# Performance work log

Measured on AMD Instinct MI355X. Metric: run time of the kernel, lower is better.

## Reference

```python
import jax, jax.numpy as jnp
import numpy as np

N, C_DEC, H, W = 16, 512, 32, 32
C_ENC, S, FEATS_IN, N_HEAD = 768, 77, 512, 8
EPS = 1e-5


def setup_inputs() -> dict:
    key = jax.random.key(0)
    ks = jax.random.split(key, 12)
    inp = {
        "input": jax.random.normal(ks[0], (N, C_DEC, H, W), jnp.float32),
        "cond": jax.random.normal(ks[1], (N, FEATS_IN), jnp.float32),
        "enc_hidden": jax.random.normal(ks[2], (N, S, C_ENC), jnp.float32),
        "enc_padding_mask": jax.random.randint(ks[3], (N, S), 0, 2).astype(jnp.float32),
        # AdaGN linear: feats_in -> 2*c_dec (scales, shifts)
        "adagn_w": jax.random.normal(ks[4], (2 * C_DEC, FEATS_IN), jnp.float32) * 0.02,
        "adagn_b": jnp.zeros((2 * C_DEC,), jnp.float32),
        # LayerNorm(c_enc) affine
        "ln_w": jnp.ones((C_ENC,), jnp.float32),
        "ln_b": jnp.zeros((C_ENC,), jnp.float32),
        # 1x1 conv q projection (treated as channel matmul)
        "q_w": jax.random.normal(ks[5], (C_DEC, C_DEC), jnp.float32) * 0.02,
        "q_b": jnp.zeros((C_DEC,), jnp.float32),
        # kv linear: c_enc -> 2*c_dec
        "kv_w": jax.random.normal(ks[6], (2 * C_DEC, C_ENC), jnp.float32) * 0.02,
        "kv_b": jnp.zeros((2 * C_DEC,), jnp.float32),
        # 1x1 conv out projection
        "out_w": jax.random.normal(ks[7], (C_DEC, C_DEC), jnp.float32) * 0.02,
        "out_b": jnp.zeros((C_DEC,), jnp.float32),
    }
    return inp


def reference(input, cond, enc_hidden, enc_padding_mask,
              adagn_w, adagn_b, ln_w, ln_b,
              q_w, q_b, kv_w, kv_b, out_w, out_b):
    n, c, h, w = input.shape
    d = c // N_HEAD

    # --- AdaGN: GroupNorm(1, c, affine=False) then cond-dependent scale/shift ---
    mu = jnp.mean(input, axis=(1, 2, 3), keepdims=True)
    var = jnp.var(input, axis=(1, 2, 3), keepdims=True)
    normed = (input - mu) * jax.lax.rsqrt(var + EPS)
    ss = cond @ adagn_w.T + adagn_b                      # [n, 2c]
    scales, shifts = ss[:, :c], ss[:, c:]
    x = shifts[:, :, None, None] + normed * (scales[:, :, None, None] + 1.0)

    # --- q projection (1x1 conv == per-pixel channel matmul) ---
    q = jnp.einsum('nchw,oc->nohw', x, q_w) + q_b[None, :, None, None]
    q = q.reshape(n, N_HEAD, d, h * w).transpose(0, 1, 3, 2)   # [n, head, hw, d]

    # --- encoder LayerNorm + kv projection ---
    mu_e = jnp.mean(enc_hidden, axis=-1, keepdims=True)
    var_e = jnp.var(enc_hidden, axis=-1, keepdims=True)
    e = (enc_hidden - mu_e) * jax.lax.rsqrt(var_e + EPS) * ln_w + ln_b
    kv = e @ kv_w.T + kv_b                               # [n, S, 2c]
    s = kv.shape[1]
    kv = kv.reshape(n, s, 2 * N_HEAD, d).transpose(0, 2, 1, 3)  # [n, 2*head, S, d]
    k, v = kv[:, :N_HEAD], kv[:, N_HEAD:]

    # --- scaled dot-product attention with additive padding mask ---
    scale = d ** (-0.25)
    att = jnp.einsum('nhqd,nhkd->nhqk', q * scale, k * scale)
    att = att - enc_padding_mask[:, None, None, :] * 10000.0
    att = jax.nn.softmax(att, axis=-1)
    y = jnp.einsum('nhqk,nhkd->nhqd', att, v)            # [n, head, hw, d]
    y = y.transpose(0, 1, 3, 2).reshape(n, c, h, w)

    out = jnp.einsum('nchw,oc->nohw', y, out_w) + out_b[None, :, None, None]
    return input + out
```

## Files before the change

### kernel.cpp

```cpp
#include <hip/hip_runtime.h>
#include <math.h>

typedef unsigned short u16;
typedef __bf16 bf16x8 __attribute__((ext_vector_type(8)));
typedef float f32x4 __attribute__((ext_vector_type(4)));

#define AS1 __attribute__((address_space(1)))
#define AS3 __attribute__((address_space(3)))

#define N_    16
#define C_    512
#define HW_   1024
#define CE_   768
#define S_    77
#define NH_   8
#define D_    64
#define FEATS_ 512
#define EPS_  1e-5f
#define TOK_  (N_ * S_)

#define WS_PSTAT 0
#define WS_QBIAS 1024
#define WSU_BYTE 131072
#define U_QW  0
#define U_OW  262144
#define U_KVW 524288
#define U_EB  1310720
#define U_KVB 2256896
#define U_QT  3518464
#define U_XT  11907072

__device__ __forceinline__ u16 f2bf(float f) {
    unsigned u = __float_as_uint(f);
    return (u16)((u + 0x7FFFu + ((u >> 16) & 1u)) >> 16);
}
__device__ __forceinline__ float bf2f(u16 h) {
    return __uint_as_float(((unsigned)h) << 16);
}

__global__ __launch_bounds__(256) void mega1_kernel(const float* __restrict__ inp,
                                                    float* __restrict__ pstats,
                                                    const float* __restrict__ qw,
                                                    const float* __restrict__ ow,
                                                    const float* __restrict__ kvw,
                                                    u16* __restrict__ uq,
                                                    u16* __restrict__ uo,
                                                    u16* __restrict__ ukv,
                                                    const float* __restrict__ enc,
                                                    const float* __restrict__ lnw,
                                                    const float* __restrict__ lnb,
                                                    u16* __restrict__ eb,
                                                    const float* __restrict__ cond,
                                                    const float* __restrict__ agw,
                                                    const float* __restrict__ agb,
                                                    float* __restrict__ ssf) {
    int bid = blockIdx.x;
    int tid = threadIdx.x;
    if (bid < 256) {
        int n = bid >> 4, slice = bid & 15;
        const float* base = inp + (size_t)n * C_ * HW_ + slice * (C_ * HW_ / 16);
        float s = 0.f, s2 = 0.f;
        const float4* b4 = (const float4*)base;
        for (int i = tid; i < (C_ * HW_ / 16) / 4; i += 256) {
            float4 v = b4[i];
            s  += v.x + v.y + v.z + v.w;
            s2 += v.x * v.x + v.y * v.y + v.z * v.z + v.w * v.w;
        }
        for (int off = 32; off; off >>= 1) {
            s  += __shfl_down(s, off);
            s2 += __shfl_down(s2, off);
        }
        __shared__ float sh[8];
        int wid = tid >> 6, lane = tid & 63;
        if (lane == 0) { sh[wid] = s; sh[4 + wid] = s2; }
        __syncthreads();
        if (tid == 0) {
            pstats[bid * 2]     = sh[0] + sh[1] + sh[2] + sh[3];
            pstats[bid * 2 + 1] = sh[4] + sh[5] + sh[6] + sh[7];
        }
    } else if (bid < 1536) {
        int i = (bid - 256) * 256 + tid;
        const float* s; u16* d; int j;
        if (i < 65536)       { s = qw;  d = uq;  j = i; }
        else if (i < 131072) { s = ow;  d = uo;  j = i - 65536; }
        else                 { s = kvw; d = ukv; j = i - 131072; }
        float4 v = ((const float4*)s)[j];
        ushort4 w;
        w.x = f2bf(v.x); w.y = f2bf(v.y); w.z = f2bf(v.z); w.w = f2bf(v.w);
        ((ushort4*)(d))[j] = w;
    } else if (bid < 2768) {
        int tok = bid - 1536;
        const float* row = enc + (size_t)tok * CE_;
        int t = tid;
        float v0 = row[t], v1 = row[t + 256], v2 = row[t + 512];
        float sum = v0 + v1 + v2;
        float sq  = v0 * v0 + v1 * v1 + v2 * v2;
        for (int off = 32; off; off >>= 1) {
            sum += __shfl_down(sum, off);
            sq  += __shfl_down(sq, off);
        }
        __shared__ float red[8];
        int wid = t >> 6, lane = t & 63;
        if (lane == 0) { red[wid] = sum; red[4 + wid] = sq; }
        __syncthreads();
        float tot = red[0] + red[1] + red[2] + red[3];
        float tsq = red[4] + red[5] + red[6] + red[7];
        float mu  = tot / CE_;
        float var = tsq / CE_ - mu * mu;
        float rstd = rsqrtf(var + EPS_);
        u16* o = eb + (size_t)tok * CE_;
        o[t]       = f2bf((v0 - mu) * rstd * lnw[t] + lnb[t]);
        o[t + 256] = f2bf((v1 - mu) * rstd * lnw[t + 256] + lnb[t + 256]);
        o[t + 512] = f2bf((v2 - mu) * rstd * lnw[t + 512] + lnb[t + 512]);
    } else {
        __shared__ float wz[16][512];
        __shared__ float cz[16][512];
        int r0 = (bid - 2768) * 16;
        for (int i = tid; i < 2048; i += 256) {
            int row = i >> 7, f4 = i & 127;
            *(float4*)&cz[row][f4 * 4] = ((const float4*)(cond + (size_t)row * 512))[f4];
            *(float4*)&wz[row][f4 * 4] = ((const float4*)(agw + (size_t)(r0 + row) * 512))[f4];
        }
        __syncthreads();
        int n = tid >> 4, r = tid & 15;
        float acc = agb[r0 + r];
        for (int i = 0; i < 128; i++) {
            int j = (r + i) & 127;
            float4 c4 = *(const float4*)&cz[n][j * 4];
            float4 w4 = *(const float4*)&wz[r][j * 4];
            acc += c4.x * w4.x + c4.y * w4.y + c4.z * w4.z + c4.w * w4.w;
        }
        ssf[(size_t)n * 1024 + r0 + r] = acc;
    }
}

__global__ __launch_bounds__(256) void mega2_kernel(const float* __restrict__ inp,
                                                    const float* __restrict__ ssf,
                                                    const float* __restrict__ pstats,
                                                    u16* __restrict__ xT,
                                                    const float* __restrict__ qw,
                                                    const float* __restrict__ qb,
                                                    float* __restrict__ qbias) {
    int bid = blockIdx.x;
    int tid = threadIdx.x;
    float cnt = (float)(C_ * HW_);
    if (bid < 2048) {
        int n = bid >> 7, rem = bid & 127;
        int c0 = (rem >> 4) * 64, h0 = (rem & 15) * 64;
        float s = 0.f, s2 = 0.f;
        for (int k = 0; k < 16; k++) {
            s  += pstats[(n * 16 + k) * 2];
            s2 += pstats[(n * 16 + k) * 2 + 1];
        }
        float mu = s / cnt;
        float rstd = rsqrtf(s2 / cnt - mu * mu + EPS_);
        __shared__ float t[64][65];
        int rr = tid >> 4, cc = (tid & 15) * 4;
#pragma unroll
        for (int i = 0; i < 4; i++) {
            int cl = rr + i * 16;
            int c = c0 + cl;
            float a = rstd * (ssf[(size_t)n * 1024 + c] + 1.f);
            float4 v = *(const float4*)(inp + ((size_t)n * C_ + c) * HW_ + h0 + cc);
            t[cl][cc + 0] = v.x * a; t[cl][cc + 1] = v.y * a;
            t[cl][cc + 2] = v.z * a; t[cl][cc + 3] = v.w * a;
        }
        __syncthreads();
#pragma unroll
        for (int i = 0; i < 4; i++) {
            int hl = rr + i * 16;
            ushort4 w;
            w.x = f2bf(t[cc + 0][hl]); w.y = f2bf(t[cc + 1][hl]);
            w.z = f2bf(t[cc + 2][hl]); w.w = f2bf(t[cc + 3][hl]);
            *(ushort4*)(xT + ((size_t)n * HW_ + h0 + hl) * C_ + c0 + cc) = w;
        }
    } else {
        __shared__ float wz[16][512];
        __shared__ float cz[16][512];
        __shared__ float muS[16], rsS[16];
        int r0 = (bid - 2048) * 16;
        if (tid < 16) {
            float s = 0.f, s2 = 0.f;
            for (int k = 0; k < 16; k++) {
                s  += pstats[(tid * 16 + k) * 2];
                s2 += pstats[(tid * 16 + k) * 2 + 1];
            }
            float mu = s / cnt;
            muS[tid] = mu;
            rsS[tid] = rsqrtf(s2 / cnt - mu * mu + EPS_);
        }
        __syncthreads();
        for (int i = tid; i < 2048; i += 256) {
            int row = i >> 7, f4 = i & 127;
            float4 sc4 = ((const float4*)(ssf + (size_t)row * 1024))[f4];
            float4 sh4 = ((const float4*)(ssf + (size_t)row * 1024 + 512))[f4];
            float mu = muS[row], rs = rsS[row];
            float4 b;
            b.x = sh4.x - mu * (rs * (sc4.x + 1.f));
            b.y = sh4.y - mu * (rs * (sc4.y + 1.f));
            b.z = sh4.z - mu * (rs * (sc4.z + 1.f));
            b.w = sh4.w - mu * (rs * (sc4.w + 1.f));
            *(float4*)&cz[row][f4 * 4] = b;
            *(float4*)&wz[row][f4 * 4] = ((const float4*)(qw + (size_t)(r0 + row) * 512))[f4];
        }
        __syncthreads();
        int n = tid >> 4, r = tid & 15;
        float acc = qb[r0 + r];
        for (int i = 0; i < 128; i++) {
            int j = (r + i) & 127;
            float4 c4 = *(const float4*)&cz[n][j * 4];
            float4 w4 = *(const float4*)&wz[r][j * 4];
            acc += c4.x * w4.x + c4.y * w4.y + c4.z * w4.z + c4.w * w4.w;
        }
        qbias[(size_t)n * 512 + r0 + r] = acc;
    }
}

__device__ __forceinline__ void gemm_mainloop(const u16* __restrict__ A, int lda, int arow0,
                                              const u16* __restrict__ B, int ldb, int brow0, int brmax,
                                              int K, f32x4 (&acc)[4][4], u16* As, u16* Bs) {
    int tid = threadIdx.x;
    int lane = tid & 63;
    int wm = ((tid >> 6) >> 1) * 64, wn = ((tid >> 6) & 1) * 64;
    int srow = tid >> 3;
    int sw = (tid & 7) ^ (srow & 7);
    int ldsoff = tid * 8;
    for (int kt = 0; kt < K; kt += 64) {
        __syncthreads();
#pragma unroll
        for (int i = 0; i < 4; i++) {
            int ar = arow0 + i * 32 + srow;
            const u16* ga = A + (size_t)ar * lda + kt + sw * 8;
            __builtin_amdgcn_global_load_lds((AS1 void*)ga, (AS3 void*)(As + i * 2048 + ldsoff), 16, 0, 0);
            int br = brow0 + i * 32 + srow; if (br > brmax) br = brmax;
            const u16* gb = B + (size_t)br * ldb + kt + sw * 8;
            __builtin_amdgcn_global_load_lds((AS1 void*)gb, (AS3 void*)(Bs + i * 2048 + ldsoff), 16, 0, 0);
        }
        __syncthreads();
#pragma unroll
        for (int kk = 0; kk < 2; kk++) {
            bf16x8 af[4], bfv[4];
            int ks = kk * 4 + (lane >> 4);
#pragma unroll
            for (int mi = 0; mi < 4; mi++) {
                int r = wm + mi * 16 + (lane & 15);
                af[mi] = *(const bf16x8*)(As + r * 64 + (ks ^ (r & 7)) * 8);
            }
#pragma unroll
            for (int ni = 0; ni < 4; ni++) {
                int r = wn + ni * 16 + (lane & 15);
                bfv[ni] = *(const bf16x8*)(Bs + r * 64 + (ks ^ (r & 7)) * 8);
            }
#pragma unroll
            for (int mi = 0; mi < 4; mi++)
#pragma unroll
                for (int ni = 0; ni < 4; ni++)
                    acc[mi][ni] = __builtin_amdgcn_mfma_f32_16x16x32_bf16(af[mi], bfv[ni], acc[mi][ni], 0, 0, 0);
        }
    }
}

__global__ __launch_bounds__(256) void mega3_kernel(const u16* __restrict__ qwb,
                                                    const u16* __restrict__ xT,
                                                    const float* __restrict__ qbias,
                                                    u16* __restrict__ qt,
                                                    const u16* __restrict__ kvwb,
                                                    const u16* __restrict__ eb,
                                                    const float* __restrict__ kvbias,
                                                    u16* __restrict__ kvo) {
    __shared__ __align__(16) u16 As[128 * 64];
    __shared__ __align__(16) u16 Bs[128 * 64];
    int bid = blockIdx.x;
    int lane = threadIdx.x & 63, wid = threadIdx.x >> 6;
    int wm = (wid >> 1) * 64, wn = (wid & 1) * 64;
    f32x4 acc[4][4];
#pragma unroll
    for (int mi = 0; mi < 4; mi++)
#pragma unroll
        for (int ni = 0; ni < 4; ni++) acc[mi][ni] = 0.f;

    if (bid < 512) {
        int n = bid >> 5, r = bid & 31;
        int brow0 = (r & 7) * 128, arow0 = (r >> 3) * 128;
        gemm_mainloop(qwb, C_, arow0, xT + (size_t)n * HW_ * C_, C_, brow0, HW_ - 1, C_, acc, As, Bs);
        u16* CT = qt + (size_t)n * HW_ * C_;
        const float* qbn = qbias + n * C_;
#pragma unroll
        for (int mi = 0; mi < 4; mi++) {
            int row = arow0 + wm + mi * 16 + ((lane >> 4) << 2);
            float4 b4 = *(const float4*)(qbn + row);
#pragma unroll
            for (int ni = 0; ni < 4; ni++) {
                int col = brow0 + wn + ni * 16 + (lane & 15);
                f32x4 v = acc[mi][ni];
                ushort4 w;
                w.x = f2bf(v.x + b4.x); w.y = f2bf(v.y + b4.y);
                w.z = f2bf(v.z + b4.z); w.w = f2bf(v.w + b4.w);
                *(ushort4*)(CT + (size_t)col * C_ + row) = w;
            }
        }
    } else {
        int t = bid - 512;
        int brow0 = (t % 10) * 128, arow0 = (t / 10) * 128;
        gemm_mainloop(kvwb, CE_, arow0, eb, CE_, brow0, TOK_ - 1, CE_, acc, As, Bs);
#pragma unroll
        for (int mi = 0; mi < 4; mi++) {
            int row = arow0 + wm + mi * 16 + ((lane >> 4) << 2);
            float4 b4 = *(const float4*)(kvbias + row);
#pragma unroll
            for (int ni = 0; ni < 4; ni++) {
                int col = brow0 + wn + ni * 16 + (lane & 15);
                if (col < TOK_) {
                    f32x4 v = acc[mi][ni];
                    ushort4 w;
                    w.x = f2bf(v.x + b4.x); w.y = f2bf(v.y + b4.y);
                    w.z = f2bf(v.z + b4.z); w.w = f2bf(v.w + b4.w);
                    *(ushort4*)(kvo + (size_t)col * 1024 + row) = w;
                }
            }
        }
    }
}

__global__ __launch_bounds__(256) void gemm_out_mfma(const u16* __restrict__ owb,
                                                     const u16* __restrict__ yT,
                                                     const float* __restrict__ ob,
                                                     const float* __restrict__ inp,
                                                     float* __restrict__ outp) {
    __shared__ __align__(16) u16 As[128 * 64];
    __shared__ __align__(16) u16 Bs[128 * 64];
    int n = blockIdx.z;
    int arow0 = blockIdx.y * 128, brow0 = blockIdx.x * 128;
    f32x4 acc[4][4];
#pragma unroll
    for (int mi = 0; mi < 4; mi++)
#pragma unroll
        for (int ni = 0; ni < 4; ni++) acc[mi][ni] = 0.f;
    gemm_mainloop(owb, C_, arow0, yT + (size_t)n * HW_ * C_, C_, brow0, HW_ - 1, C_, acc, As, Bs);
    int lane = threadIdx.x & 63, wid = threadIdx.x >> 6;
    int wm = (wid >> 1) * 64, wn = (wid & 1) * 64;
    float* Co = outp + (size_t)n * C_ * HW_;
    const float* In = inp + (size_t)n * C_ * HW_;
#pragma unroll
    for (int mi = 0; mi < 4; mi++) {
        int row = arow0 + wm + mi * 16 + ((lane >> 4) << 2);
        float4 b4 = *(const float4*)(ob + row);
#pragma unroll
        for (int ni = 0; ni < 4; ni++) {
            int col = brow0 + wn + ni * 16 + (lane & 15);
            f32x4 v = acc[mi][ni];
            size_t i0 = (size_t)row * HW_ + col;
            Co[i0]            = v.x + b4.x + In[i0];
            Co[i0 + HW_]      = v.y + b4.y + In[i0 + HW_];
            Co[i0 + 2 * HW_]  = v.z + b4.z + In[i0 + 2 * HW_];
            Co[i0 + 3 * HW_]  = v.w + b4.w + In[i0 + 3 * HW_];
        }
    }
}

__global__ __launch_bounds__(256) void attn_mfma(const u16* __restrict__ kvb,
                                                 const float* __restrict__ mask,
                                                 const u16* __restrict__ qt,
                                                 u16* __restrict__ yt) {
    int nh = blockIdx.x;
    int n = nh >> 3, h = nh & 7;
    int qb = blockIdx.y;
    __shared__ __align__(16) u16 Qs[64 * 64];
    __shared__ __align__(16) u16 Ks[80 * 64];
    __shared__ __align__(16) u16 VT[64 * 104];
    __shared__ __align__(16) u16 Ps[64 * 104];
    __shared__ float msk[80];
    int tid = threadIdx.x;
    int lane = tid & 63, w = tid >> 6;
    int g = lane >> 4, l15 = lane & 15;

    const u16* qbase = qt + ((size_t)(n * HW_ + qb * 64)) * C_ + h * 64;
#pragma unroll
    for (int pass = 0; pass < 2; pass++) {
        int idx = pass * 256 + tid;
        int row = idx >> 3, slot = idx & 7;
        int sw = slot ^ (row & 7);
        __builtin_amdgcn_global_load_lds((AS1 void*)(qbase + (size_t)row * C_ + sw * 8),
                                         (AS3 void*)(Qs + idx * 8), 16, 0, 0);
    }
    const u16* kbase = kvb + (size_t)(n * S_) * 1024 + h * 64;
#pragma unroll
    for (int pass = 0; pass < 3; pass++) {
        int idx = pass * 256 + tid;
        if (idx < 640) {
            int row = idx >> 3, slot = idx & 7;
            int srow = row < S_ ? row : S_ - 1;
            int sw = slot ^ (row & 7);
            __builtin_amdgcn_global_load_lds((AS1 void*)(kbase + (size_t)srow * 1024 + sw * 8),
                                             (AS3 void*)(Ks + idx * 8), 16, 0, 0);
        }
    }
    {
        int d = tid & 63, sg = tid >> 6;
        const u16* vbase = kvb + (size_t)(n * S_) * 1024 + 512 + h * 64 + d;
        for (int s = sg; s < 104; s += 4) {
            u16 v = (s < S_) ? vbase[(size_t)s * 1024] : (u16)0;
            VT[d * 104 + s] = v;
        }
    }
    for (int i = tid; i < 512; i += 256) {
        int r = i >> 3, cp = i & 7;
        *(unsigned*)&Ps[r * 104 + 80 + cp * 2] = 0u;
    }
    if (tid < 80) msk[tid] = (tid < S_) ? mask[n * S_ + tid] * 10000.f : 0.f;
    __syncthreads();

    int qrow = w * 16 + l15;

    bf16x8 qf[2];
#pragma unroll
    for (int kk = 0; kk < 2; kk++) {
        int s8 = kk * 4 + g;
        qf[kk] = *(const bf16x8*)(Qs + qrow * 64 + (s8 ^ (qrow & 7)) * 8);
    }
    f32x4 sc[5];
#pragma unroll
    for (int kb = 0; kb < 5; kb++) {
        sc[kb] = 0.f;
#pragma unroll
        for (int kk = 0; kk < 2; kk++) {
            int r = kb * 16 + l15;
            int s8 = kk * 4 + g;
            bf16x8 kf = *(const bf16x8*)(Ks + r * 64 + (s8 ^ (r & 7)) * 8);
            sc[kb] = __builtin_amdgcn_mfma_f32_16x16x32_bf16(kf, qf[kk], sc[kb], 0, 0, 0);
        }
    }
    float sv[5][4];
    float mx = -3e38f;
#pragma unroll
    for (int kb = 0; kb < 5; kb++)
#pragma unroll
        for (int j = 0; j < 4; j++) {
            int key = kb * 16 + g * 4 + j;
            float s = sc[kb][j] * 0.125f - msk[key];
            sv[kb][j] = s;
            if (key < S_) mx = fmaxf(mx, s);
        }
    mx = fmaxf(mx, __shfl_xor(mx, 16));
    mx = fmaxf(mx, __shfl_xor(mx, 32));
    float sum = 0.f;
    float p[5][4];
#pragma unroll
    for (int kb = 0; kb < 5; kb++)
#pragma unroll
        for (int j = 0; j < 4; j++) {
            int key = kb * 16 + g * 4 + j;
            float pv = (key < S_) ? __expf(sv[kb][j] - mx) : 0.f;
            p[kb][j] = pv;
            sum += pv;
        }
    sum += __shfl_xor(sum, 16);
    sum += __shfl_xor(sum, 32);
    float inv = 1.f / sum;
#pragma unroll
    for (int kb = 0; kb < 5; kb++) {
        unsigned lo = (unsigned)f2bf(p[kb][0] * inv) | ((unsigned)f2bf(p[kb][1] * inv) << 16);
        unsigned hi = (unsigned)f2bf(p[kb][2] * inv) | ((unsigned)f2bf(p[kb][3] * inv) << 16);
        int col = kb * 16 + g * 4;
        *(uint2*)&Ps[qrow * 104 + col] = make_uint2(lo, hi);
    }
    f32x4 ya[4];
#pragma unroll
    for (int mf = 0; mf < 4; mf++) ya[mf] = 0.f;
#pragma unroll
    for (int kk = 0; kk < 3; kk++) {
        int s8 = kk * 4 + g;
        bf16x8 pf = *(const bf16x8*)(Ps + qrow * 104 + s8 * 8);
#pragma unroll
        for (int mf = 0; mf < 4; mf++) {
            bf16x8 vf = *(const bf16x8*)(VT + (mf * 16 + l15) * 104 + s8 * 8);
            ya[mf] = __builtin_amdgcn_mfma_f32_16x16x32_bf16(vf, pf, ya[mf], 0, 0, 0);
        }
    }
    u16* yrow = yt + ((size_t)(n * HW_ + qb * 64 + qrow)) * C_ + h * 64;
#pragma unroll
    for (int mf = 0; mf < 4; mf++) {
        int d0 = mf * 16 + g * 4;
        ushort4 o;
        o.x = f2bf(ya[mf][0]); o.y = f2bf(ya[mf][1]);
        o.z = f2bf(ya[mf][2]); o.w = f2bf(ya[mf][3]);
        *(ushort4*)(yrow + d0) = o;
    }
}

extern "C" void kernel_launch(void* const* d_in, const int* in_sizes, int n_in,
                              void* d_out, int out_size, void* d_ws, size_t ws_size,
                              hipStream_t stream) {
    const float* inp  = (const float*)d_in[0];
    const float* cond = (const float*)d_in[1];
    const float* enc  = (const float*)d_in[2];
    const float* mask = (const float*)d_in[3];
    const float* agw  = (const float*)d_in[4];
    const float* agb  = (const float*)d_in[5];
    const float* lnw  = (const float*)d_in[6];
    const float* lnb  = (const float*)d_in[7];
    const float* qw   = (const float*)d_in[8];
    const float* qb   = (const float*)d_in[9];
    const float* kvw  = (const float*)d_in[10];
    const float* kvb  = (const float*)d_in[11];
    const float* ow   = (const float*)d_in[12];
    const float* ob   = (const float*)d_in[13];
    float* ws  = (float*)d_ws;
    float* out = (float*)d_out;
    u16* wsu = (u16*)((char*)d_ws + WSU_BYTE);
    float* ssf = (float*)(wsu + U_QT);

    mega1_kernel<<<dim3(2832), 256, 0, stream>>>(inp, ws + WS_PSTAT,
                                                 qw, ow, kvw, wsu + U_QW, wsu + U_OW, wsu + U_KVW,
                                                 enc, lnw, lnb, wsu + U_EB,
                                                 cond, agw, agb, ssf);
    mega2_kernel<<<dim3(2080), 256, 0, stream>>>(inp, ssf, ws + WS_PSTAT,
                                                 wsu + U_XT, qw, qb, ws + WS_QBIAS);
    mega3_kernel<<<dim3(592), 256, 0, stream>>>(wsu + U_QW, wsu + U_XT, ws + WS_QBIAS, wsu + U_QT,
                                                wsu + U_KVW, wsu + U_EB, kvb, wsu + U_KVB);

    attn_mfma<<<dim3(N_ * NH_, HW_ / 64), 256, 0, stream>>>(
        wsu + U_KVB, mask, wsu + U_QT, wsu + U_XT);

    gemm_out_mfma<<<dim3(HW_ / 128, C_ / 128, N_), 256, 0, stream>>>(
        wsu + U_OW, wsu + U_XT, ob, inp, out);
}
```

Baseline: 111.8 us.

## Fold AdaGN scale into per-batch q weights, transpose raw input earlier

The per-channel AdaGN scale (rstd*(scale+1)) is moved out of the input transpose and folded into a per-batch copy of the q-projection weight, so the bf16 transpose of the raw input can run in the first kernel alongside the statistics pass instead of waiting for them. The second kernel becomes small: it builds 16 scaled bf16 weight matrices plus the bias terms. This shortens the dependency chain and turns a large streaming pass into a small weight pass. In exchange the q GEMM reads per-batch weights instead of one shared matrix, which adds workspace traffic, and mega1 now reserves 64KB of shared memory in every block, which may reduce its occupancy.

New measurement: 113.6 us. Within noise of the previous version (+1.6%).

```diff
diff --git a/kernel.cpp b/kernel.cpp
--- a/kernel.cpp
+++ b/kernel.cpp
@@ -22,28 +22,24 @@
 #define WS_PSTAT 0
 #define WS_QBIAS 1024
 #define WSU_BYTE 131072
-#define U_QW  0
 #define U_OW  262144
 #define U_KVW 524288
 #define U_EB  1310720
 #define U_KVB 2256896
 #define U_QT  3518464
 #define U_XT  11907072
+#define U_QWA 20295680
 
 __device__ __forceinline__ u16 f2bf(float f) {
     unsigned u = __float_as_uint(f);
     return (u16)((u + 0x7FFFu + ((u >> 16) & 1u)) >> 16);
 }
-__device__ __forceinline__ float bf2f(u16 h) {
-    return __uint_as_float(((unsigned)h) << 16);
-}
 
 __global__ __launch_bounds__(256) void mega1_kernel(const float* __restrict__ inp,
                                                     float* __restrict__ pstats,
-                                                    const float* __restrict__ qw,
+                                                    u16* __restrict__ xT,
                                                     const float* __restrict__ ow,
                                                     const float* __restrict__ kvw,
-                                                    u16* __restrict__ uq,
                                                     u16* __restrict__ uo,
                                                     u16* __restrict__ ukv,
                                                     const float* __restrict__ enc,
@@ -54,6 +50,7 @@
                                                     const float* __restrict__ agw,
                                                     const float* __restrict__ agb,
                                                     float* __restrict__ ssf) {
+    __shared__ __align__(16) float smem[16384];
     int bid = blockIdx.x;
     int tid = threadIdx.x;
     if (bid < 256) {
@@ -70,26 +67,47 @@
             s  += __shfl_down(s, off);
             s2 += __shfl_down(s2, off);
         }
-        __shared__ float sh[8];
         int wid = tid >> 6, lane = tid & 63;
-        if (lane == 0) { sh[wid] = s; sh[4 + wid] = s2; }
+        if (lane == 0) { smem[wid] = s; smem[4 + wid] = s2; }
         __syncthreads();
         if (tid == 0) {
-            pstats[bid * 2]     = sh[0] + sh[1] + sh[2] + sh[3];
-            pstats[bid * 2 + 1] = sh[4] + sh[5] + sh[6] + sh[7];
-        }
-    } else if (bid < 1536) {
-        int i = (bid - 256) * 256 + tid;
+            pstats[bid * 2]     = smem[0] + smem[1] + smem[2] + smem[3];
+            pstats[bid * 2 + 1] = smem[4] + smem[5] + smem[6] + smem[7];
+        }
+    } else if (bid < 2304) {
+        int bid2 = bid - 256;
+        int n = bid2 >> 7, rem = bid2 & 127;
+        int c0 = (rem >> 4) * 64, h0 = (rem & 15) * 64;
+        float (*t)[65] = (float(*)[65])smem;
+        int rr = tid >> 4, cc = (tid & 15) * 4;
+#pragma unroll
+        for (int i = 0; i < 4; i++) {
+            int cl = rr + i * 16;
+            int c = c0 + cl;
+            float4 v = *(const float4*)(inp + ((size_t)n * C_ + c) * HW_ + h0 + cc);
+            t[cl][cc + 0] = v.x; t[cl][cc + 1] = v.y;
+            t[cl][cc + 2] = v.z; t[cl][cc + 3] = v.w;
+        }
+        __syncthreads();
+#pragma unroll
+        for (int i = 0; i < 4; i++) {
+            int hl = rr + i * 16;
+            ushort4 w;
+            w.x = f2bf(t[cc + 0][hl]); w.y = f2bf(t[cc + 1][hl]);
+            w.z = f2bf(t[cc + 2][hl]); w.w = f2bf(t[cc + 3][hl]);
+            *(ushort4*)(xT + ((size_t)n * HW_ + h0 + hl) * C_ + c0 + cc) = w;
+        }
+    } else if (bid < 3328) {
+        int i = (bid - 2304) * 256 + tid;
         const float* s; u16* d; int j;
-        if (i < 65536)       { s = qw;  d = uq;  j = i; }
-        else if (i < 131072) { s = ow;  d = uo;  j = i - 65536; }
-        else                 { s = kvw; d = ukv; j = i - 131072; }
+        if (i < 65536) { s = ow;  d = uo;  j = i; }
+        else           { s = kvw; d = ukv; j = i - 65536; }
         float4 v = ((const float4*)s)[j];
         ushort4 w;
         w.x = f2bf(v.x); w.y = f2bf(v.y); w.z = f2bf(v.z); w.w = f2bf(v.w);
         ((ushort4*)(d))[j] = w;
-    } else if (bid < 2768) {
-        int tok = bid - 1536;
+    } else if (bid < 4560) {
+        int tok = bid - 3328;
         const float* row = enc + (size_t)tok * CE_;
         int t = tid;
         float v0 = row[t], v1 = row[t + 256], v2 = row[t + 512];
@@ -99,12 +117,11 @@
             sum += __shfl_down(sum, off);
             sq  += __shfl_down(sq, off);
         }
-        __shared__ float red[8];
         int wid = t >> 6, lane = t & 63;
-        if (lane == 0) { red[wid] = sum; red[4 + wid] = sq; }
-        __syncthreads();
-        float tot = red[0] + red[1] + red[2] + red[3];
-        float tsq = red[4] + red[5] + red[6] + red[7];
+        if (lane == 0) { smem[wid] = sum; smem[4 + wid] = sq; }
+        __syncthreads();
+        float tot = smem[0] + smem[1] + smem[2] + smem[3];
+        float tsq = smem[4] + smem[5] + smem[6] + smem[7];
         float mu  = tot / CE_;
         float var = tsq / CE_ - mu * mu;
         float rstd = rsqrtf(var + EPS_);
@@ -113,9 +130,9 @@
         o[t + 256] = f2bf((v1 - mu) * rstd * lnw[t + 256] + lnb[t + 256]);
         o[t + 512] = f2bf((v2 - mu) * rstd * lnw[t + 512] + lnb[t + 512]);
     } else {
-        __shared__ float wz[16][512];
-        __shared__ float cz[16][512];
-        int r0 = (bid - 2768) * 16;
+        float (*wz)[512] = (float(*)[512])smem;
+        float (*cz)[512] = (float(*)[512])(smem + 8192);
+        int r0 = (bid - 4560) * 16;
         for (int i = tid; i < 2048; i += 256) {
             int row = i >> 7, f4 = i & 127;
             *(float4*)&cz[row][f4 * 4] = ((const float4*)(cond + (size_t)row * 512))[f4];
@@ -134,19 +151,19 @@
     }
 }
 
-__global__ __launch_bounds__(256) void mega2_kernel(const float* __restrict__ inp,
-                                                    const float* __restrict__ ssf,
+__global__ __launch_bounds__(256) void mega2_kernel(const float* __restrict__ ssf,
                                                     const float* __restrict__ pstats,
-                                                    u16* __restrict__ xT,
                                                     const float* __restrict__ qw,
+                                                    u16* __restrict__ qwa,
                                                     const float* __restrict__ qb,
                                                     float* __restrict__ qbias) {
+    __shared__ __align__(16) float smem[16384];
+    __shared__ float muS[16], rsS[16];
     int bid = blockIdx.x;
     int tid = threadIdx.x;
     float cnt = (float)(C_ * HW_);
-    if (bid < 2048) {
-        int n = bid >> 7, rem = bid & 127;
-        int c0 = (rem >> 4) * 64, h0 = (rem & 15) * 64;
+    if (bid < 256) {
+        int n = bid >> 4, o0 = (bid & 15) * 32;
         float s = 0.f, s2 = 0.f;
         for (int k = 0; k < 16; k++) {
             s  += pstats[(n * 16 + k) * 2];
@@ -154,31 +171,24 @@
         }
         float mu = s / cnt;
         float rstd = rsqrtf(s2 / cnt - mu * mu + EPS_);
-        __shared__ float t[64][65];
-        int rr = tid >> 4, cc = (tid & 15) * 4;
-#pragma unroll
-        for (int i = 0; i < 4; i++) {
-            int cl = rr + i * 16;
-            int c = c0 + cl;
-            float a = rstd * (ssf[(size_t)n * 1024 + c] + 1.f);
-            float4 v = *(const float4*)(inp + ((size_t)n * C_ + c) * HW_ + h0 + cc);
-            t[cl][cc + 0] = v.x * a; t[cl][cc + 1] = v.y * a;
-            t[cl][cc + 2] = v.z * a; t[cl][cc + 3] = v.w * a;
-        }
-        __syncthreads();
-#pragma unroll
-        for (int i = 0; i < 4; i++) {
-            int hl = rr + i * 16;
+        float* al = smem;
+        for (int c = tid; c < 512; c += 256)
+            al[c] = rstd * (ssf[(size_t)n * 1024 + c] + 1.f);
+        __syncthreads();
+        u16* dst = qwa + (size_t)n * 262144;
+        for (int i = tid; i < 4096; i += 256) {
+            int o = i >> 7, f4 = i & 127;
+            float4 w4 = ((const float4*)(qw + (size_t)(o0 + o) * 512))[f4];
+            int c = f4 * 4;
             ushort4 w;
-            w.x = f2bf(t[cc + 0][hl]); w.y = f2bf(t[cc + 1][hl]);
-            w.z = f2bf(t[cc + 2][hl]); w.w = f2bf(t[cc + 3][hl]);
-            *(ushort4*)(xT + ((size_t)n * HW_ + h0 + hl) * C_ + c0 + cc) = w;
+            w.x = f2bf(w4.x * al[c]);     w.y = f2bf(w4.y * al[c + 1]);
+            w.z = f2bf(w4.z * al[c + 2]); w.w = f2bf(w4.w * al[c + 3]);
+            *(ushort4*)(dst + (size_t)(o0 + o) * 512 + c) = w;
         }
     } else {
-        __shared__ float wz[16][512];
-        __shared__ float cz[16][512];
-        __shared__ float muS[16], rsS[16];
-        int r0 = (bid - 2048) * 16;
+        float (*wz)[512] = (float(*)[512])smem;
+        float (*cz)[512] = (float(*)[512])(smem + 8192);
+        int r0 = (bid - 256) * 16;
         if (tid < 16) {
             float s = 0.f, s2 = 0.f;
             for (int k = 0; k < 16; k++) {
@@ -260,7 +270,7 @@
     }
 }
 
-__global__ __launch_bounds__(256) void mega3_kernel(const u16* __restrict__ qwb,
+__global__ __launch_bounds__(256) void mega3_kernel(const u16* __restrict__ qwa,
                                                     const u16* __restrict__ xT,
                                                     const float* __restrict__ qbias,
                                                     u16* __restrict__ qt,
@@ -282,7 +292,8 @@
     if (bid < 512) {
         int n = bid >> 5, r = bid & 31;
         int brow0 = (r & 7) * 128, arow0 = (r >> 3) * 128;
-        gemm_mainloop(qwb, C_, arow0, xT + (size_t)n * HW_ * C_, C_, brow0, HW_ - 1, C_, acc, As, Bs);
+        gemm_mainloop(qwa + (size_t)n * 262144, C_, arow0,
+                      xT + (size_t)n * HW_ * C_, C_, brow0, HW_ - 1, C_, acc, As, Bs);
         u16* CT = qt + (size_t)n * HW_ * C_;
         const float* qbn = qbias + n * C_;
 #pragma unroll
@@ -510,13 +521,13 @@
     u16* wsu = (u16*)((char*)d_ws + WSU_BYTE);
     float* ssf = (float*)(wsu + U_QT);
 
-    mega1_kernel<<<dim3(2832), 256, 0, stream>>>(inp, ws + WS_PSTAT,
-                                                 qw, ow, kvw, wsu + U_QW, wsu + U_OW, wsu + U_KVW,
+    mega1_kernel<<<dim3(4624), 256, 0, stream>>>(inp, ws + WS_PSTAT, wsu + U_XT,
+                                                 ow, kvw, wsu + U_OW, wsu + U_KVW,
                                                  enc, lnw, lnb, wsu + U_EB,
                                                  cond, agw, agb, ssf);
-    mega2_kernel<<<dim3(2080), 256, 0, stream>>>(inp, ssf, ws + WS_PSTAT,
-                                                 wsu + U_XT, qw, qb, ws + WS_QBIAS);
-    mega3_kernel<<<dim3(592), 256, 0, stream>>>(wsu + U_QW, wsu + U_XT, ws + WS_QBIAS, wsu + U_QT,
+    mega2_kernel<<<dim3(288), 256, 0, stream>>>(ssf, ws + WS_PSTAT, qw,
+                                                wsu + U_QWA, qb, ws + WS_QBIAS);
+    mega3_kernel<<<dim3(592), 256, 0, stream>>>(wsu + U_QWA, wsu + U_XT, ws + WS_QBIAS, wsu + U_QT,
                                                 wsu + U_KVW, wsu + U_EB, kvb, wsu + U_KVB);
 
     attn_mfma<<<dim3(N_ * NH_, HW_ / 64), 256, 0, stream>>>(
```

## Reuse K/V tiles across four query blocks per attention workgroup

Applied to the files above, without the earlier changes.

The attention kernel now loops over four 64-row query blocks per workgroup, so K, V and the mask are loaded into LDS once and reused instead of being reloaded for every query block. The grid shrinks from 16 to 4 blocks in y. The branch-specific shared arrays in the two setup kernels are merged into one shared buffer, which lowers their LDS footprint. The attention change trades parallelism (2048 to 512 workgroups) and adds barriers per iteration for less redundant K/V traffic.

New measurement: 102.0 us. -8.7%, faster.

```diff
diff --git a/kernel.cpp b/kernel.cpp
--- a/kernel.cpp
+++ b/kernel.cpp
@@ -33,9 +33,6 @@
 __device__ __forceinline__ u16 f2bf(float f) {
     unsigned u = __float_as_uint(f);
     return (u16)((u + 0x7FFFu + ((u >> 16) & 1u)) >> 16);
-}
-__device__ __forceinline__ float bf2f(u16 h) {
-    return __uint_as_float(((unsigned)h) << 16);
 }
 
 __global__ __launch_bounds__(256) void mega1_kernel(const float* __restrict__ inp,
@@ -54,6 +51,7 @@
                                                     const float* __restrict__ agw,
                                                     const float* __restrict__ agb,
                                                     float* __restrict__ ssf) {
+    __shared__ __align__(16) float smem[16384];
     int bid = blockIdx.x;
     int tid = threadIdx.x;
     if (bid < 256) {
@@ -70,13 +68,12 @@
             s  += __shfl_down(s, off);
             s2 += __shfl_down(s2, off);
         }
-        __shared__ float sh[8];
         int wid = tid >> 6, lane = tid & 63;
-        if (lane == 0) { sh[wid] = s; sh[4 + wid] = s2; }
+        if (lane == 0) { smem[wid] = s; smem[4 + wid] = s2; }
         __syncthreads();
         if (tid == 0) {
-            pstats[bid * 2]     = sh[0] + sh[1] + sh[2] + sh[3];
-            pstats[bid * 2 + 1] = sh[4] + sh[5] + sh[6] + sh[7];
+            pstats[bid * 2]     = smem[0] + smem[1] + smem[2] + smem[3];
+            pstats[bid * 2 + 1] = smem[4] + smem[5] + smem[6] + smem[7];
         }
     } else if (bid < 1536) {
         int i = (bid - 256) * 256 + tid;
@@ -99,12 +96,11 @@
             sum += __shfl_down(sum, off);
             sq  += __shfl_down(sq, off);
         }
-        __shared__ float red[8];
         int wid = t >> 6, lane = t & 63;
-        if (lane == 0) { red[wid] = sum; red[4 + wid] = sq; }
-        __syncthreads();
-        float tot = red[0] + red[1] + red[2] + red[3];
-        float tsq = red[4] + red[5] + red[6] + red[7];
+        if (lane == 0) { smem[wid] = sum; smem[4 + wid] = sq; }
+        __syncthreads();
+        float tot = smem[0] + smem[1] + smem[2] + smem[3];
+        float tsq = smem[4] + smem[5] + smem[6] + smem[7];
         float mu  = tot / CE_;
         float var = tsq / CE_ - mu * mu;
         float rstd = rsqrtf(var + EPS_);
@@ -113,8 +109,8 @@
         o[t + 256] = f2bf((v1 - mu) * rstd * lnw[t + 256] + lnb[t + 256]);
         o[t + 512] = f2bf((v2 - mu) * rstd * lnw[t + 512] + lnb[t + 512]);
     } else {
-        __shared__ float wz[16][512];
-        __shared__ float cz[16][512];
+        float (*wz)[512] = (float(*)[512])smem;
+        float (*cz)[512] = (float(*)[512])(smem + 8192);
         int r0 = (bid - 2768) * 16;
         for (int i = tid; i < 2048; i += 256) {
             int row = i >> 7, f4 = i & 127;
@@ -141,6 +137,8 @@
                                                     const float* __restrict__ qw,
                                                     const float* __restrict__ qb,
                                                     float* __restrict__ qbias) {
+    __shared__ __align__(16) float smem[16384];
+    __shared__ float muS[16], rsS[16];
     int bid = blockIdx.x;
     int tid = threadIdx.x;
     float cnt = (float)(C_ * HW_);
@@ -154,7 +152,7 @@
         }
         float mu = s / cnt;
         float rstd = rsqrtf(s2 / cnt - mu * mu + EPS_);
-        __shared__ float t[64][65];
+        float (*t)[65] = (float(*)[65])smem;
         int rr = tid >> 4, cc = (tid & 15) * 4;
 #pragma unroll
         for (int i = 0; i < 4; i++) {
@@ -175,9 +173,8 @@
             *(ushort4*)(xT + ((size_t)n * HW_ + h0 + hl) * C_ + c0 + cc) = w;
         }
     } else {
-        __shared__ float wz[16][512];
-        __shared__ float cz[16][512];
-        __shared__ float muS[16], rsS[16];
+        float (*wz)[512] = (float(*)[512])smem;
+        float (*cz)[512] = (float(*)[512])(smem + 8192);
         int r0 = (bid - 2048) * 16;
         if (tid < 16) {
             float s = 0.f, s2 = 0.f;
@@ -364,7 +361,6 @@
                                                  u16* __restrict__ yt) {
     int nh = blockIdx.x;
     int n = nh >> 3, h = nh & 7;
-    int qb = blockIdx.y;
     __shared__ __align__(16) u16 Qs[64 * 64];
     __shared__ __align__(16) u16 Ks[80 * 64];
     __shared__ __align__(16) u16 VT[64 * 104];
@@ -374,15 +370,6 @@
     int lane = tid & 63, w = tid >> 6;
     int g = lane >> 4, l15 = lane & 15;
 
-    const u16* qbase = qt + ((size_t)(n * HW_ + qb * 64)) * C_ + h * 64;
-#pragma unroll
-    for (int pass = 0; pass < 2; pass++) {
-        int idx = pass * 256 + tid;
-        int row = idx >> 3, slot = idx & 7;
-        int sw = slot ^ (row & 7);
-        __builtin_amdgcn_global_load_lds((AS1 void*)(qbase + (size_t)row * C_ + sw * 8),
-                                         (AS3 void*)(Qs + idx * 8), 16, 0, 0);
-    }
     const u16* kbase = kvb + (size_t)(n * S_) * 1024 + h * 64;
 #pragma unroll
     for (int pass = 0; pass < 3; pass++) {
@@ -408,83 +395,97 @@
         *(unsigned*)&Ps[r * 104 + 80 + cp * 2] = 0u;
     }
     if (tid < 80) msk[tid] = (tid < S_) ? mask[n * S_ + tid] * 10000.f : 0.f;
-    __syncthreads();
 
     int qrow = w * 16 + l15;
 
-    bf16x8 qf[2];
-#pragma unroll
-    for (int kk = 0; kk < 2; kk++) {
-        int s8 = kk * 4 + g;
-        qf[kk] = *(const bf16x8*)(Qs + qrow * 64 + (s8 ^ (qrow & 7)) * 8);
-    }
-    f32x4 sc[5];
-#pragma unroll
-    for (int kb = 0; kb < 5; kb++) {
-        sc[kb] = 0.f;
+    for (int qi = 0; qi < 4; qi++) {
+        int qb = blockIdx.y * 4 + qi;
+        __syncthreads();
+        const u16* qbase = qt + ((size_t)(n * HW_ + qb * 64)) * C_ + h * 64;
+#pragma unroll
+        for (int pass = 0; pass < 2; pass++) {
+            int idx = pass * 256 + tid;
+            int row = idx >> 3, slot = idx & 7;
+            int sw = slot ^ (row & 7);
+            __builtin_amdgcn_global_load_lds((AS1 void*)(qbase + (size_t)row * C_ + sw * 8),
+                                             (AS3 void*)(Qs + idx * 8), 16, 0, 0);
+        }
+        __syncthreads();
+
+        bf16x8 qf[2];
 #pragma unroll
         for (int kk = 0; kk < 2; kk++) {
-            int r = kb * 16 + l15;
             int s8 = kk * 4 + g;
-            bf16x8 kf = *(const bf16x8*)(Ks + r * 64 + (s8 ^ (r & 7)) * 8);
-            sc[kb] = __builtin_amdgcn_mfma_f32_16x16x32_bf16(kf, qf[kk], sc[kb], 0, 0, 0);
-        }
-    }
-    float sv[5][4];
-    float mx = -3e38f;
-#pragma unroll
-    for (int kb = 0; kb < 5; kb++)
-#pragma unroll
-        for (int j = 0; j < 4; j++) {
-            int key = kb * 16 + g * 4 + j;
-            float s = sc[kb][j] * 0.125f - msk[key];
-            sv[kb][j] = s;
-            if (key < S_) mx = fmaxf(mx, s);
-        }
-    mx = fmaxf(mx, __shfl_xor(mx, 16));
-    mx = fmaxf(mx, __shfl_xor(mx, 32));
-    float sum = 0.f;
-    float p[5][4];
-#pragma unroll
-    for (int kb = 0; kb < 5; kb++)
-#pragma unroll
-        for (int j = 0; j < 4; j++) {
-            int key = kb * 16 + g * 4 + j;
-            float pv = (key < S_) ? __expf(sv[kb][j] - mx) : 0.f;
-            p[kb][j] = pv;
-            sum += pv;
-        }
-    sum += __shfl_xor(sum, 16);
-    sum += __shfl_xor(sum, 32);
-    float inv = 1.f / sum;
-#pragma unroll
-    for (int kb = 0; kb < 5; kb++) {
-        unsigned lo = (unsigned)f2bf(p[kb][0] * inv) | ((unsigned)f2bf(p[kb][1] * inv) << 16);
-        unsigned hi = (unsigned)f2bf(p[kb][2] * inv) | ((unsigned)f2bf(p[kb][3] * inv) << 16);
-        int col = kb * 16 + g * 4;
-        *(uint2*)&Ps[qrow * 104 + col] = make_uint2(lo, hi);
-    }
-    f32x4 ya[4];
-#pragma unroll
-    for (int mf = 0; mf < 4; mf++) ya[mf] = 0.f;
-#pragma unroll
-    for (int kk = 0; kk < 3; kk++) {
-        int s8 = kk * 4 + g;
-        bf16x8 pf = *(const bf16x8*)(Ps + qrow * 104 + s8 * 8);
+            qf[kk] = *(const bf16x8*)(Qs + qrow * 64 + (s8 ^ (qrow & 7)) * 8);
+        }
+        f32x4 sc[5];
+#pragma unroll
+        for (int kb = 0; kb < 5; kb++) {
+            sc[kb] = 0.f;
+#pragma unroll
+            for (int kk = 0; kk < 2; kk++) {
+                int r = kb * 16 + l15;
+                int s8 = kk * 4 + g;
+                bf16x8 kf = *(const bf16x8*)(Ks + r * 64 + (s8 ^ (r & 7)) * 8);
+                sc[kb] = __builtin_amdgcn_mfma_f32_16x16x32_bf16(kf, qf[kk], sc[kb], 0, 0, 0);
+            }
+        }
+        float sv[5][4];
+        float mx = -3e38f;
+#pragma unroll
+        for (int kb = 0; kb < 5; kb++)
+#pragma unroll
+            for (int j = 0; j < 4; j++) {
+                int key = kb * 16 + g * 4 + j;
+                float s = sc[kb][j] * 0.125f - msk[key];
+                sv[kb][j] = s;
+                if (key < S_) mx = fmaxf(mx, s);
+            }
+        mx = fmaxf(mx, __shfl_xor(mx, 16));
+        mx = fmaxf(mx, __shfl_xor(mx, 32));
+        float sum = 0.f;
+        float p[5][4];
+#pragma unroll
+        for (int kb = 0; kb < 5; kb++)
+#pragma unroll
+            for (int j = 0; j < 4; j++) {
+                int key = kb * 16 + g * 4 + j;
+                float pv = (key < S_) ? __expf(sv[kb][j] - mx) : 0.f;
+                p[kb][j] = pv;
+                sum += pv;
+            }
+        sum += __shfl_xor(sum, 16);
+        sum += __shfl_xor(sum, 32);
+        float inv = 1.f / sum;
+#pragma unroll
+        for (int kb = 0; kb < 5; kb++) {
+            unsigned lo = (unsigned)f2bf(p[kb][0] * inv) | ((unsigned)f2bf(p[kb][1] * inv) << 16);
+            unsigned hi = (unsigned)f2bf(p[kb][2] * inv) | ((unsigned)f2bf(p[kb][3] * inv) << 16);
+            int col = kb * 16 + g * 4;
+            *(uint2*)&Ps[qrow * 104 + col] = make_uint2(lo, hi);
+        }
+        f32x4 ya[4];
+#pragma unroll
+        for (int mf = 0; mf < 4; mf++) ya[mf] = 0.f;
+#pragma unroll
+        for (int kk = 0; kk < 3; kk++) {
+            int s8 = kk * 4 + g;
+            bf16x8 pf = *(const bf16x8*)(Ps + qrow * 104 + s8 * 8);
+#pragma unroll
+            for (int mf = 0; mf < 4; mf++) {
+                bf16x8 vf = *(const bf16x8*)(VT + (mf * 16 + l15) * 104 + s8 * 8);
+                ya[mf] = __builtin_amdgcn_mfma_f32_16x16x32_bf16(vf, pf, ya[mf], 0, 0, 0);
+            }
+        }
+        u16* yrow = yt + ((size_t)(n * HW_ + qb * 64 + qrow)) * C_ + h * 64;
 #pragma unroll
         for (int mf = 0; mf < 4; mf++) {
-            bf16x8 vf = *(const bf16x8*)(VT + (mf * 16 + l15) * 104 + s8 * 8);
-            ya[mf] = __builtin_amdgcn_mfma_f32_16x16x32_bf16(vf, pf, ya[mf], 0, 0, 0);
-        }
-    }
-    u16* yrow = yt + ((size_t)(n * HW_ + qb * 64 + qrow)) * C_ + h * 64;
-#pragma unroll
-    for (int mf = 0; mf < 4; mf++) {
-        int d0 = mf * 16 + g * 4;
-        ushort4 o;
-        o.x = f2bf(ya[mf][0]); o.y = f2bf(ya[mf][1]);
-        o.z = f2bf(ya[mf][2]); o.w = f2bf(ya[mf][3]);
-        *(ushort4*)(yrow + d0) = o;
+            int d0 = mf * 16 + g * 4;
+            ushort4 o;
+            o.x = f2bf(ya[mf][0]); o.y = f2bf(ya[mf][1]);
+            o.z = f2bf(ya[mf][2]); o.w = f2bf(ya[mf][3]);
+            *(ushort4*)(yrow + d0) = o;
+        }
     }
 }
 
@@ -519,7 +520,7 @@
     mega3_kernel<<<dim3(592), 256, 0, stream>>>(wsu + U_QW, wsu + U_XT, ws + WS_QBIAS, wsu + U_QT,
                                                 wsu + U_KVW, wsu + U_EB, kvb, wsu + U_KVB);
 
-    attn_mfma<<<dim3(N_ * NH_, HW_ / 64), 256, 0, stream>>>(
+    attn_mfma<<<dim3(N_ * NH_, 4), 256, 0, stream>>>(
         wsu + U_KVB, mask, wsu + U_QT, wsu + U_XT);
 
     gemm_out_mfma<<<dim3(HW_ / 128, C_ / 128, N_), 256, 0, stream>>>(
```
